# Kernel tuning notes

Measured on AMD Instinct MI355X. Metric: run time of the kernel, lower is better.

The kernel has to match this reference:

```python
import jax, jax.numpy as jnp
import numpy as np

B, C, H, W = 16, 256, 128, 128
INTER = C // 2  # NLBlockND default inter_channels = in_channels // 2
BN_EPS = 1e-5


def setup_inputs() -> dict:
    key = jax.random.key(0)
    ks = jax.random.split(key, 14)
    s = lambda n: 1.0 / np.sqrt(n)
    inp = {
        'x':  jax.random.normal(ks[0], (B, C, H, W), jnp.float32),
        # NLBlockND 1x1 convs (spatial input is 1x1 after avg-pool -> matmuls)
        'Wg': jax.random.normal(ks[1], (INTER, C), jnp.float32) * s(C),
        'bg': jax.random.normal(ks[2], (INTER,), jnp.float32) * s(C),
        'Wt': jax.random.normal(ks[3], (INTER, C), jnp.float32) * s(C),
        'bt': jax.random.normal(ks[4], (INTER,), jnp.float32) * s(C),
        'Wp': jax.random.normal(ks[5], (INTER, C), jnp.float32) * s(C),
        'bp': jax.random.normal(ks[6], (INTER,), jnp.float32) * s(C),
        'Wf': jax.random.normal(ks[7], (1, 2 * INTER), jnp.float32) * s(2 * INTER),
        'bf': jax.random.normal(ks[8], (1,), jnp.float32) * s(2 * INTER),
        'Wz': jax.random.normal(ks[9], (C, INTER), jnp.float32) * s(INTER),
        'bz': jax.random.normal(ks[10], (C,), jnp.float32) * s(INTER),
        'gamma': jax.random.normal(ks[11], (C,), jnp.float32),
        'beta':  jax.random.normal(ks[12], (C,), jnp.float32),
        # eca_layer_two: Conv2d(C, 1, kernel_size=1, bias=False)
        'W3': jax.random.normal(ks[13], (1, C), jnp.float32) * s(C),
    }
    return inp


def reference(x, Wg, bg, Wt, bt, Wp, bp, Wf, bf, Wz, bz, gamma, beta, W3):
    b = x.shape[0]
    # ---- nonlocal_layer: avg-pool -> NLBlockND('concatenate') on 1x1 map ----
    p = jnp.mean(x, axis=(2, 3))                      # [b, C] pooled vector
    g_x = p @ Wg.T + bg                               # [b, INTER]
    th  = p @ Wt.T + bt                               # theta  [b, INTER]
    ph  = p @ Wp.T + bp                               # phi    [b, INTER]
    cat = jnp.concatenate([th, ph], axis=1)           # [b, 2*INTER]
    f = jax.nn.relu(cat @ Wf.T + bf)                  # [b, 1]; N=1 so f_div_C = f
    y = f * g_x                                       # [b, INTER]
    wy = y @ Wz.T + bz                                # [b, C]
    # BatchNorm2d (training mode, spatial=1x1): stats over batch per channel
    mu = jnp.mean(wy, axis=0)
    var = jnp.var(wy, axis=0)
    bn = gamma * (wy - mu) * jax.lax.rsqrt(var + BN_EPS) + beta
    z = bn + p                                        # residual
    scores = jax.nn.sigmoid(z)                        # [b, C]
    # top-3 channel selection, then per-sample gather of channels from x
    _, idx = jax.lax.top_k(scores, 3)                 # [b, 3]
    x1 = jnp.take_along_axis(x, idx[:, :, None, None], axis=1)  # [b, 3, H, W]
    # ---- eca_layer_two: 1x1 conv C->1 (no bias) + exact GELU ----
    x3 = jax.nn.gelu(jnp.einsum('bchw,oc->bohw', x, W3), approximate=False)  # [b,1,H,W]
    # conv2 (eca_layer_one) output is discarded (x2 = zeros_like, unused)
    return jnp.concatenate([x3, x1], axis=1)          # [b, 4, H, W]
```

## Files before the change

### kernel.cpp

```cpp
#include <hip/hip_runtime.h>

#define HW    16384
#define NCH   256
#define NB    16
#define INTER 128
#define HW4   4096
#define WSTR  34


__global__ __launch_bounds__(512, 2) void k_pool_x3(
    const float* __restrict__ x, const float* __restrict__ W3, float* out)
{
    const int tile = blockIdx.x;
    const int b    = blockIdx.y;
    const int tid  = threadIdx.x;
    const int wave = tid >> 6, lane = tid & 63;
    const int c0   = wave << 5;

    __shared__ float  w3f[NCH];
    __shared__ float  wsum[NCH * WSTR];
    __shared__ float4 comb[7][256];

    if (tid < NCH) w3f[tid] = W3[tid];
    __syncthreads();

    const float4* xb = (const float4*)x + (size_t)b * NCH * HW4
                     + (size_t)c0 * HW4 + tile * 256 + lane;

    float4 a[4];
    #pragma unroll
    for (int q = 0; q < 4; ++q) a[q] = make_float4(0.f, 0.f, 0.f, 0.f);

    float4 bufA[8], bufB[8];
    #pragma unroll
    for (int j = 0; j < 8; ++j)
        bufA[j] = xb[(size_t)(j >> 2) * HW4 + (j & 3) * 64];

    #define PROCESS(BUF, CBASE)                                             \
        _Pragma("unroll")                                                   \
        for (int h = 0; h < 2; ++h) {                                       \
            const int c = (CBASE) + h;                                      \
            const float w = w3f[c0 + c];                                    \
            float cs = 0.f;                                                 \
            _Pragma("unroll")                                               \
            for (int q = 0; q < 4; ++q) {                                   \
                float4 v = BUF[h * 4 + q];                                  \
                a[q].x = fmaf(v.x, w, a[q].x);                              \
                a[q].y = fmaf(v.y, w, a[q].y);                              \
                a[q].z = fmaf(v.z, w, a[q].z);                              \
                a[q].w = fmaf(v.w, w, a[q].w);                              \
                cs += (v.x + v.y) + (v.z + v.w);                            \
            }                                                               \
            cs += __shfl_xor(cs, 32);                                       \
            if (lane < 32) wsum[(c0 + c) * WSTR + lane] = cs;               \
        }

    for (int cc = 0; cc < 32; cc += 4) {
        #pragma unroll
        for (int j = 0; j < 8; ++j)
            bufB[j] = xb[(size_t)(cc + 2 + (j >> 2)) * HW4 + (j & 3) * 64];
        PROCESS(bufA, cc)
        if (cc + 4 < 32) {
            #pragma unroll
            for (int j = 0; j < 8; ++j)
                bufA[j] = xb[(size_t)(cc + 4 + (j >> 2)) * HW4 + (j & 3) * 64];
        }
        PROCESS(bufB, cc + 2)
    }
    #undef PROCESS

    __syncthreads();

    {
        const int ch = tid >> 1, half = tid & 1;
        const float* rowp = &wsum[ch * WSTR + half * 16];
        float s = 0.f;
        #pragma unroll
        for (int k = 0; k < 8; ++k) {
            float2 v2 = *(const float2*)(rowp + k * 2);
            s += v2.x + v2.y;
        }
        s += __shfl_xor(s, 1);
        if (half == 0)
            out[(size_t)(b * 4 + 1) * HW + tile * NCH + ch] = s;
    }

    if (wave > 0) {
        #pragma unroll
        for (int q = 0; q < 4; ++q) comb[wave - 1][q * 64 + lane] = a[q];
    }
    __syncthreads();
    if (wave == 0) {
        #pragma unroll
        for (int j = 0; j < 7; ++j) {
            #pragma unroll
            for (int q = 0; q < 4; ++q) {
                float4 v = comb[j][q * 64 + lane];
                a[q].x += v.x; a[q].y += v.y; a[q].z += v.z; a[q].w += v.w;
            }
        }
        const float is2 = 0.70710678118654752440f;
        #pragma unroll
        for (int q = 0; q < 4; ++q) {
            float4 r;
            r.x = 0.5f * a[q].x * (1.f + erff(a[q].x * is2));
            r.y = 0.5f * a[q].y * (1.f + erff(a[q].y * is2));
            r.z = 0.5f * a[q].z * (1.f + erff(a[q].z * is2));
            r.w = 0.5f * a[q].w * (1.f + erff(a[q].w * is2));
            ((float4*)out)[(size_t)b * 4 * HW4 + tile * 256 + q * 64 + lane] = r;
        }
    }
}

__global__ __launch_bounds__(256) void k_mlp(
    const float* outbuf,
    const float* __restrict__ Wg, const float* __restrict__ bg,
    const float* __restrict__ Wt, const float* __restrict__ bt,
    const float* __restrict__ Wp, const float* __restrict__ bp,
    const float* __restrict__ Wf, const float* __restrict__ bfv,
    const float* __restrict__ Wz, const float* __restrict__ bz,
    float* __restrict__ p_out, float* __restrict__ wy_out)
{
    const int b = blockIdx.x, tid = threadIdx.x;
    __shared__ float sp[NCH];
    __shared__ float sg[INTER], sth[INTER], sph[INTER];
    __shared__ float red[NCH];
    __shared__ float sy[INTER];
    __shared__ float sf;

    const float* psum = outbuf + (size_t)(b * 4 + 1) * HW;
    float s = 0.f;
    #pragma unroll
    for (int t = 0; t < 16; ++t) s += psum[t * NCH + tid];
    float pv = s * (1.0f / 16384.0f);
    sp[tid] = pv;
    p_out[b * NCH + tid] = pv;
    __syncthreads();

    for (int j = tid; j < 3 * INTER; j += 256) {
        const float* Wrow; float bias; int i, which;
        if (j < INTER)        { i = j;           Wrow = Wg + i * NCH; bias = bg[i]; which = 0; }
        else if (j < 2*INTER) { i = j - INTER;   Wrow = Wt + i * NCH; bias = bt[i]; which = 1; }
        else                  { i = j - 2*INTER; Wrow = Wp + i * NCH; bias = bp[i]; which = 2; }
        float acc = bias;
        for (int k = 0; k < NCH; k += 4) {
            float4 q = *(const float4*)(Wrow + k);
            acc = fmaf(q.x, sp[k+0], acc);
            acc = fmaf(q.y, sp[k+1], acc);
            acc = fmaf(q.z, sp[k+2], acc);
            acc = fmaf(q.w, sp[k+3], acc);
        }
        if (which == 0) sg[i] = acc;
        else if (which == 1) sth[i] = acc;
        else sph[i] = acc;
    }
    __syncthreads();

    float cat = (tid < INTER) ? sth[tid] : sph[tid - INTER];
    red[tid] = cat * Wf[tid];
    __syncthreads();
    if (tid == 0) {
        float acc = bfv[0];
        for (int k = 0; k < NCH; ++k) acc += red[k];
        sf = fmaxf(acc, 0.f);
    }
    __syncthreads();
    if (tid < INTER) sy[tid] = sf * sg[tid];
    __syncthreads();

    {
        const float* Wrow = Wz + tid * INTER;
        float acc = bz[tid];
        for (int k = 0; k < INTER; k += 4) {
            float4 q = *(const float4*)(Wrow + k);
            acc = fmaf(q.x, sy[k+0], acc);
            acc = fmaf(q.y, sy[k+1], acc);
            acc = fmaf(q.z, sy[k+2], acc);
            acc = fmaf(q.w, sy[k+3], acc);
        }
        wy_out[b * NCH + tid] = acc;
    }
}

__global__ __launch_bounds__(256) void k_bn_topk(
    const float* __restrict__ wy, const float* __restrict__ p,
    const float* __restrict__ gamma, const float* __restrict__ beta,
    int* __restrict__ sel_out)
{
    const int b = blockIdx.x, tid = threadIdx.x;
    const int wave = tid >> 6, lane = tid & 63;
    __shared__ float wsc[4];
    __shared__ int   wid[4];
    __shared__ int   sel[3];

    float vv[16];
    float mu = 0.f;
    #pragma unroll
    for (int bb = 0; bb < 16; ++bb) { vv[bb] = wy[bb * NCH + tid]; mu += vv[bb]; }
    mu *= (1.f / 16.f);
    float var = 0.f;
    #pragma unroll
    for (int bb = 0; bb < 16; ++bb) { float d = vv[bb] - mu; var = fmaf(d, d, var); }
    var *= (1.f / 16.f);

    float bn = gamma[tid] * (vv[b] - mu) * rsqrtf(var + 1e-5f) + beta[tid];
    float z  = bn + p[b * NCH + tid];
    float sc = 1.f / (1.f + expf(-z));

    for (int r = 0; r < 3; ++r) {
        float s = sc; int id = tid;
        #pragma unroll
        for (int m = 1; m <= 32; m <<= 1) {
            float so = __shfl_xor(s, m);
            int   io = __shfl_xor(id, m);
            if (so > s || (so == s && io < id)) { s = so; id = io; }
        }
        if (lane == 0) { wsc[wave] = s; wid[wave] = id; }
        __syncthreads();
        if (tid == 0) {
            float bs = wsc[0]; int bi = wid[0];
            for (int w = 1; w < 4; ++w)
                if (wsc[w] > bs || (wsc[w] == bs && wid[w] < bi)) { bs = wsc[w]; bi = wid[w]; }
            sel[r] = bi;
        }
        __syncthreads();
        if (tid == sel[r]) sc = -1e30f;
        __syncthreads();
    }
    if (tid < 3) sel_out[b * 3 + tid] = sel[tid];
}

__global__ __launch_bounds__(256) void k_gather(
    const float* __restrict__ x, const int* __restrict__ sel,
    float* __restrict__ out)
{
    const int seg = blockIdx.x;
    const int r   = blockIdx.y;
    const int b   = blockIdx.z;
    const int ch  = sel[b * 3 + r];
    const float4* src = (const float4*)x + (size_t)(b * NCH + ch) * HW4 + seg * 1024;
    float4*       dst = (float4*)out + (size_t)(b * 4 + 1 + r) * HW4 + seg * 1024;
    #pragma unroll
    for (int i = 0; i < 4; ++i)
        dst[i * 256 + threadIdx.x] = src[i * 256 + threadIdx.x];
}

extern "C" void kernel_launch(void* const* d_in, const int* in_sizes, int n_in,
                              void* d_out, int out_size, void* d_ws, size_t ws_size,
                              hipStream_t stream)
{
    const float* x     = (const float*)d_in[0];
    const float* Wg    = (const float*)d_in[1];
    const float* bg    = (const float*)d_in[2];
    const float* Wt    = (const float*)d_in[3];
    const float* bt    = (const float*)d_in[4];
    const float* Wp    = (const float*)d_in[5];
    const float* bp    = (const float*)d_in[6];
    const float* Wf    = (const float*)d_in[7];
    const float* bfv   = (const float*)d_in[8];
    const float* Wz    = (const float*)d_in[9];
    const float* bz    = (const float*)d_in[10];
    const float* gamma = (const float*)d_in[11];
    const float* beta  = (const float*)d_in[12];
    const float* W3    = (const float*)d_in[13];
    float* out = (float*)d_out;

    float* wy  = (float*)d_ws;
    float* p   = wy + NB * NCH;
    int*   sel = (int*)(p + NB * NCH);

    k_pool_x3<<<dim3(16, 16), 512, 0, stream>>>(x, W3, out);
    k_mlp<<<NB, 256, 0, stream>>>(out, Wg, bg, Wt, bt, Wp, bp, Wf, bfv, Wz, bz, p, wy);
    k_bn_topk<<<NB, 256, 0, stream>>>(wy, p, gamma, beta, sel);
    k_gather<<<dim3(4, 3, NB), 256, 0, stream>>>(x, sel, out);
}
```

Measured before the change: 396.1 us.

## Halve spatial tile per block to double grid size and raise occupancy

The pool+conv kernel now has each block cover 512 pixels instead of 1024. That doubles the grid to 32x16 blocks, and the per-thread accumulator drops from four float4 to two, with four channels per buffer stage instead of two. The cross-wave reduction is restructured so all eight waves write partials to shared memory and 128 threads finish the sum and GELU, and launch bounds now request 4 blocks per CU. The aim is more blocks in flight and lower register pressure so the memory-bound streaming of x hides latency better. In exchange there are twice as many partial pool sums for the MLP kernel to reduce, plus more per-block overhead.

```diff
diff --git a/kernel.cpp b/kernel.cpp
--- a/kernel.cpp
+++ b/kernel.cpp
@@ -6,9 +6,10 @@
 #define INTER 128
 #define HW4   4096
 #define WSTR  34
-
-
-__global__ __launch_bounds__(512, 2) void k_pool_x3(
+#define NT    32
+
+
+__global__ __launch_bounds__(512, 4) void k_pool_x3(
     const float* __restrict__ x, const float* __restrict__ W3, float* out)
 {
     const int tile = blockIdx.x;
@@ -19,56 +20,54 @@
 
     __shared__ float  w3f[NCH];
     __shared__ float  wsum[NCH * WSTR];
-    __shared__ float4 comb[7][256];
+    __shared__ float4 comb[8][128];
 
     if (tid < NCH) w3f[tid] = W3[tid];
     __syncthreads();
 
     const float4* xb = (const float4*)x + (size_t)b * NCH * HW4
-                     + (size_t)c0 * HW4 + tile * 256 + lane;
-
-    float4 a[4];
-    #pragma unroll
-    for (int q = 0; q < 4; ++q) a[q] = make_float4(0.f, 0.f, 0.f, 0.f);
+                     + (size_t)c0 * HW4 + tile * 128 + lane;
+
+    float4 a0 = make_float4(0.f, 0.f, 0.f, 0.f);
+    float4 a1 = make_float4(0.f, 0.f, 0.f, 0.f);
 
     float4 bufA[8], bufB[8];
     #pragma unroll
     for (int j = 0; j < 8; ++j)
-        bufA[j] = xb[(size_t)(j >> 2) * HW4 + (j & 3) * 64];
+        bufA[j] = xb[(size_t)(j >> 1) * HW4 + (j & 1) * 64];
 
     #define PROCESS(BUF, CBASE)                                             \
         _Pragma("unroll")                                                   \
-        for (int h = 0; h < 2; ++h) {                                       \
+        for (int h = 0; h < 4; ++h) {                                       \
             const int c = (CBASE) + h;                                      \
             const float w = w3f[c0 + c];                                    \
-            float cs = 0.f;                                                 \
-            _Pragma("unroll")                                               \
-            for (int q = 0; q < 4; ++q) {                                   \
-                float4 v = BUF[h * 4 + q];                                  \
-                a[q].x = fmaf(v.x, w, a[q].x);                              \
-                a[q].y = fmaf(v.y, w, a[q].y);                              \
-                a[q].z = fmaf(v.z, w, a[q].z);                              \
-                a[q].w = fmaf(v.w, w, a[q].w);                              \
-                cs += (v.x + v.y) + (v.z + v.w);                            \
-            }                                                               \
+            float4 v0 = BUF[h * 2], v1 = BUF[h * 2 + 1];                    \
+            a0.x = fmaf(v0.x, w, a0.x); a0.y = fmaf(v0.y, w, a0.y);         \
+            a0.z = fmaf(v0.z, w, a0.z); a0.w = fmaf(v0.w, w, a0.w);         \
+            a1.x = fmaf(v1.x, w, a1.x); a1.y = fmaf(v1.y, w, a1.y);         \
+            a1.z = fmaf(v1.z, w, a1.z); a1.w = fmaf(v1.w, w, a1.w);         \
+            float cs = ((v0.x + v0.y) + (v0.z + v0.w))                      \
+                     + ((v1.x + v1.y) + (v1.z + v1.w));                     \
             cs += __shfl_xor(cs, 32);                                       \
             if (lane < 32) wsum[(c0 + c) * WSTR + lane] = cs;               \
         }
 
-    for (int cc = 0; cc < 32; cc += 4) {
+    for (int cc = 0; cc < 32; cc += 8) {
         #pragma unroll
         for (int j = 0; j < 8; ++j)
-            bufB[j] = xb[(size_t)(cc + 2 + (j >> 2)) * HW4 + (j & 3) * 64];
+            bufB[j] = xb[(size_t)(cc + 4 + (j >> 1)) * HW4 + (j & 1) * 64];
         PROCESS(bufA, cc)
-        if (cc + 4 < 32) {
+        if (cc + 8 < 32) {
             #pragma unroll
             for (int j = 0; j < 8; ++j)
-                bufA[j] = xb[(size_t)(cc + 4 + (j >> 2)) * HW4 + (j & 3) * 64];
-        }
-        PROCESS(bufB, cc + 2)
+                bufA[j] = xb[(size_t)(cc + 8 + (j >> 1)) * HW4 + (j & 1) * 64];
+        }
+        PROCESS(bufB, cc + 4)
     }
     #undef PROCESS
 
+    comb[wave][lane]      = a0;
+    comb[wave][64 + lane] = a1;
     __syncthreads();
 
     {
@@ -85,30 +84,20 @@
             out[(size_t)(b * 4 + 1) * HW + tile * NCH + ch] = s;
     }
 
-    if (wave > 0) {
-        #pragma unroll
-        for (int q = 0; q < 4; ++q) comb[wave - 1][q * 64 + lane] = a[q];
-    }
-    __syncthreads();
-    if (wave == 0) {
-        #pragma unroll
-        for (int j = 0; j < 7; ++j) {
-            #pragma unroll
-            for (int q = 0; q < 4; ++q) {
-                float4 v = comb[j][q * 64 + lane];
-                a[q].x += v.x; a[q].y += v.y; a[q].z += v.z; a[q].w += v.w;
-            }
+    if (tid < 128) {
+        float4 v = comb[0][tid];
+        #pragma unroll
+        for (int j = 1; j < 8; ++j) {
+            float4 u = comb[j][tid];
+            v.x += u.x; v.y += u.y; v.z += u.z; v.w += u.w;
         }
         const float is2 = 0.70710678118654752440f;
-        #pragma unroll
-        for (int q = 0; q < 4; ++q) {
-            float4 r;
-            r.x = 0.5f * a[q].x * (1.f + erff(a[q].x * is2));
-            r.y = 0.5f * a[q].y * (1.f + erff(a[q].y * is2));
-            r.z = 0.5f * a[q].z * (1.f + erff(a[q].z * is2));
-            r.w = 0.5f * a[q].w * (1.f + erff(a[q].w * is2));
-            ((float4*)out)[(size_t)b * 4 * HW4 + tile * 256 + q * 64 + lane] = r;
-        }
+        float4 r;
+        r.x = 0.5f * v.x * (1.f + erff(v.x * is2));
+        r.y = 0.5f * v.y * (1.f + erff(v.y * is2));
+        r.z = 0.5f * v.z * (1.f + erff(v.z * is2));
+        r.w = 0.5f * v.w * (1.f + erff(v.w * is2));
+        ((float4*)out)[(size_t)b * 4 * HW4 + tile * 128 + tid] = r;
     }
 }
 
@@ -131,7 +120,7 @@
     const float* psum = outbuf + (size_t)(b * 4 + 1) * HW;
     float s = 0.f;
     #pragma unroll
-    for (int t = 0; t < 16; ++t) s += psum[t * NCH + tid];
+    for (int t = 0; t < NT; ++t) s += psum[t * NCH + tid];
     float pv = s * (1.0f / 16384.0f);
     sp[tid] = pv;
     p_out[b * NCH + tid] = pv;
@@ -269,7 +258,7 @@
     float* p   = wy + NB * NCH;
     int*   sel = (int*)(p + NB * NCH);
 
-    k_pool_x3<<<dim3(16, 16), 512, 0, stream>>>(x, W3, out);
+    k_pool_x3<<<dim3(NT, 16), 512, 0, stream>>>(x, W3, out);
     k_mlp<<<NB, 256, 0, stream>>>(out, Wg, bg, Wt, bt, Wp, bp, Wf, bfv, Wz, bz, p, wy);
     k_bn_topk<<<NB, 256, 0, stream>>>(wy, p, gamma, beta, sel);
     k_gather<<<dim3(4, 3, NB), 256, 0, stream>>>(x, sel, out);
```

Measured after the change: 492.5 us. +24.3%, slower.
